# Kernel tuning notes

Hardware: AMD Instinct MI355X
Metric: run time of the kernel (lower is better)

## Reference

```python
import jax, jax.numpy as jnp
import numpy as np

B, N, F_IN, H = 1, 4096, 256, 4
OUT_F = 256
HEAD_DIM = OUT_F // H
E_RAND = 131072  # avg degree 32
LN_EPS = 1e-5


def setup_inputs() -> dict:
    key = jax.random.key(0)
    ks = jax.random.split(key, 12)
    x = jax.random.normal(ks[0], (B, N, F_IN), jnp.float32)
    # random edges + self-loops so every softmax row has at least one unmasked entry
    src = jax.random.randint(ks[1], (E_RAND,), 0, N, dtype=jnp.int32)
    dst = jax.random.randint(ks[2], (E_RAND,), 0, N, dtype=jnp.int32)
    loops = jnp.arange(N, dtype=jnp.int32)
    edge_index = jnp.stack([jnp.concatenate([loops, src]), jnp.concatenate([loops, dst])])
    s = 1.0 / np.sqrt(F_IN)
    Wq = jax.random.uniform(ks[3], (OUT_F, F_IN), jnp.float32, -s, s)
    bq = jax.random.uniform(ks[4], (OUT_F,), jnp.float32, -s, s)
    Wk = jax.random.uniform(ks[5], (OUT_F, F_IN), jnp.float32, -s, s)
    bk = jax.random.uniform(ks[6], (OUT_F,), jnp.float32, -s, s)
    Wv = jax.random.uniform(ks[7], (OUT_F, F_IN), jnp.float32, -s, s)
    bv = jax.random.uniform(ks[8], (OUT_F,), jnp.float32, -s, s)
    ln_g = jnp.ones((OUT_F,), jnp.float32)
    ln_b = jnp.zeros((OUT_F,), jnp.float32)
    return {"x": x, "edge_index": edge_index, "Wq": Wq, "bq": bq, "Wk": Wk,
            "bk": bk, "Wv": Wv, "bv": bv, "ln_g": ln_g, "ln_b": ln_b}


def _layer_norm(y, g, b):
    mu = jnp.mean(y, axis=-1, keepdims=True)
    var = jnp.mean(jnp.square(y - mu), axis=-1, keepdims=True)
    return (y - mu) * jax.lax.rsqrt(var + LN_EPS) * g + b


def reference(x, edge_index, Wq, bq, Wk, bk, Wv, bv, ln_g, ln_b):
    b, n, f_in = x.shape
    out_f = Wq.shape[0]
    hd = out_f // H
    # linear projections -> [b, H, n, hd]
    Q = (x @ Wq.T + bq).reshape(b, n, H, hd).transpose(0, 2, 1, 3)
    K = (x @ Wk.T + bk).reshape(b, n, H, hd).transpose(0, 2, 1, 3)
    V = (x @ Wv.T + bv).reshape(b, n, H, hd).transpose(0, 2, 1, 3)
    scores = jnp.einsum('bhnd,bhmd->bhnm', Q, K) / jnp.sqrt(jnp.float32(hd))
    # adjacency mask: same for every batch/head (torch scatters identically per b,h)
    adj = jnp.zeros((n, n), bool).at[edge_index[0], edge_index[1]].set(True)
    scores = jnp.where(adj, scores, -jnp.inf)
    attn = jax.nn.softmax(scores, axis=-1)  # dropout = identity (eval)
    out = jnp.einsum('bhnm,bhmd->bhnd', attn, V)
    out = out.transpose(0, 2, 1, 3).reshape(b, n, out_f)
    out = out + x if f_in == out_f else out  # residual
    out = _layer_norm(out, ln_g, ln_b)
    return (out, attn)
```

## Files before the change

### kernel.cpp

```cpp
#include <hip/hip_runtime.h>
#include <stdint.h>

#define NNODES 4096
#define FDIM 256
#define NH 4
#define HD 64
#define MWORDS 128
#define SCAP 512
#define TOTROWS (NH * NNODES)
#define ROW4 (NNODES / 4)
#define R0 5120
#define R1 13824
#define NFB 2048

typedef float f4 __attribute__((ext_vector_type(4)));

__device__ __forceinline__ void fill_zero(f4* __restrict__ attn4, size_t beg, size_t end,
                                          int fid, int t)
{
    f4 z = {0.f, 0.f, 0.f, 0.f};
    size_t stride = (size_t)NFB * 256;
    for (size_t i = beg + (size_t)fid * 256 + t; i < end; i += stride)
        attn4[i] = z;
}

__global__ __launch_bounds__(256) void k_transpose_w(
    const float* __restrict__ Wq, const float* __restrict__ Wk,
    const float* __restrict__ Wv, float* __restrict__ Wt)
{
    __shared__ float tile[32][33];
    int mat = blockIdx.z;
    const float* W = mat == 0 ? Wq : (mat == 1 ? Wk : Wv);
    float* dst = Wt + (size_t)mat * FDIM * FDIM;
    int r0 = blockIdx.y * 32, c0 = blockIdx.x * 32;
    int tx = threadIdx.x, ty = threadIdx.y;
    for (int i = ty; i < 32; i += 8)
        tile[i][tx] = W[(size_t)(r0 + i) * FDIM + c0 + tx];
    __syncthreads();
    for (int i = ty; i < 32; i += 8)
        dst[(size_t)(c0 + i) * FDIM + r0 + tx] = tile[tx][i];
}

__global__ void k_mask_build(const int* __restrict__ ei, int E, uint32_t* __restrict__ mask)
{
    int e = blockIdx.x * 256 + threadIdx.x;
    if (e >= E) return;
    int r = ei[e];
    int c = ei[E + e];
    atomicOr(&mask[(size_t)r * MWORDS + (c >> 5)], 1u << (c & 31));
}

#define TN 16
__global__ __launch_bounds__(256) void k_qkv_fill(
    const float* __restrict__ x, const float* __restrict__ Wt,
    const float* __restrict__ bq, const float* __restrict__ bk, const float* __restrict__ bv,
    float* __restrict__ qkv, float* __restrict__ attn)
{
    int t = threadIdx.x;
    if (blockIdx.x >= 3 * (NNODES / TN)) {
        fill_zero((f4*)attn, 0, (size_t)R0 * ROW4, blockIdx.x - 3 * (NNODES / TN), t);
        return;
    }
    int mat = blockIdx.x >> 8;
    int n0 = (blockIdx.x & 255) * TN;
    const float* W = Wt + (size_t)mat * FDIM * FDIM;
    const float* bias = mat == 0 ? bq : (mat == 1 ? bk : bv);
    float* dst = qkv + (size_t)mat * NNODES * FDIM;
    __shared__ float xl[TN][FDIM + 4];
    for (int f = t; f < TN * (FDIM / 4); f += 256) {
        int n = f >> 6, c4 = f & 63;
        float4 v = ((const float4*)(x + (size_t)(n0 + n) * FDIM))[c4];
        *(float4*)&xl[n][c4 * 4] = v;
    }
    __syncthreads();
    float acc[TN];
    #pragma unroll
    for (int n = 0; n < TN; ++n) acc[n] = 0.f;
    for (int k4 = 0; k4 < FDIM / 4; ++k4) {
        float w0 = W[(size_t)(k4 * 4 + 0) * FDIM + t];
        float w1 = W[(size_t)(k4 * 4 + 1) * FDIM + t];
        float w2 = W[(size_t)(k4 * 4 + 2) * FDIM + t];
        float w3 = W[(size_t)(k4 * 4 + 3) * FDIM + t];
        #pragma unroll
        for (int n = 0; n < TN; ++n) {
            float4 xv = *(const float4*)&xl[n][k4 * 4];
            acc[n] = fmaf(w0, xv.x, acc[n]);
            acc[n] = fmaf(w1, xv.y, acc[n]);
            acc[n] = fmaf(w2, xv.z, acc[n]);
            acc[n] = fmaf(w3, xv.w, acc[n]);
        }
    }
    float bb = bias[t];
    #pragma unroll
    for (int n = 0; n < TN; ++n)
        dst[(size_t)(n0 + n) * FDIM + t] = acc[n] + bb;
}

__global__ __launch_bounds__(256) void k_attn_fill(
    const float* __restrict__ qkv, const uint32_t* __restrict__ mask,
    const float* __restrict__ x, const float* __restrict__ ln_g, const float* __restrict__ ln_b,
    float* __restrict__ out, float* __restrict__ stats, float* __restrict__ attn)
{
    int t = threadIdx.x;
    if (blockIdx.x >= NNODES) {
        fill_zero((f4*)attn, (size_t)R0 * ROW4, (size_t)R1 * ROW4, blockIdx.x - NNODES, t);
        return;
    }

    const float* Q = qkv;
    const float* K = qkv + (size_t)NNODES * FDIM;
    const float* V = qkv + 2 * (size_t)NNODES * FDIM;

    __shared__ float q_lds[FDIM];
    __shared__ uint32_t mrow[MWORDS];
    __shared__ unsigned short list[NNODES];
    __shared__ float sv[NH][SCAP];
    __shared__ float red0[NH], red1[NH];
    __shared__ int cnt_s;

    int n = blockIdx.x;
    int h = t >> 6, lane = t & 63;

    q_lds[t] = Q[(size_t)n * FDIM + t];
    float xv = x[(size_t)n * FDIM + t];
    if (t < MWORDS) mrow[t] = mask[(size_t)n * MWORDS + t];
    __syncthreads();

    if (t < 64) {
        int total = 0;
        for (int r = 0; r < 2; ++r) {
            int w = r * 64 + t;
            uint32_t bits = mrow[w];
            int c = __popc(bits);
            int scan = c;
            #pragma unroll
            for (int off = 1; off < 64; off <<= 1) {
                int u = __shfl_up(scan, off);
                if (t >= off) scan += u;
            }
            int base = total + scan - c;
            while (bits) {
                int b = __ffs(bits) - 1;
                list[base++] = (unsigned short)(w * 32 + b);
                bits &= bits - 1;
            }
            total += __shfl(scan, 63);
        }
        if (t == 0) cnt_s = total;
    }
    __syncthreads();
    int cnt = cnt_s;

    const float4* qh = (const float4*)(q_lds + h * HD);

    float mi = -INFINITY, li = 0.f;
    for (int i = lane; i < cnt; i += 64) {
        int m = list[i];
        const float4* kp = (const float4*)(K + (size_t)m * FDIM + h * HD);
        float s = 0.f;
        #pragma unroll
        for (int j = 0; j < HD / 4; ++j) {
            float4 a = qh[j], b = kp[j];
            s += a.x * b.x + a.y * b.y + a.z * b.z + a.w * b.w;
        }
        s *= 0.125f;
        if (i < SCAP) sv[h][i] = s;
        float nm = fmaxf(mi, s);
        li = li * __expf(mi - nm) + __expf(s - nm);
        mi = nm;
    }
    #pragma unroll
    for (int off = 32; off; off >>= 1) {
        float mo = __shfl_xor(mi, off);
        float lo = __shfl_xor(li, off);
        float nm = fmaxf(mi, mo);
        float ea = (nm == -INFINITY) ? 0.f : __expf(mi - nm);
        float eb = (nm == -INFINITY) ? 0.f : __expf(mo - nm);
        li = li * ea + lo * eb;
        mi = nm;
    }
    float M = mi;
    float Linv = 1.f / li;
    if (lane == 0) {
        stats[((size_t)h * NNODES + n) * 2 + 0] = M;
        stats[((size_t)h * NNODES + n) * 2 + 1] = Linv;
    }

    int cm = min(cnt, SCAP);
    for (int i = lane; i < cm; i += 64)
        sv[h][i] = __expf(sv[h][i] - M) * Linv;

    const float* vb = V + (size_t)h * HD + lane;
    float o0 = 0.f, o1 = 0.f, o2 = 0.f, o3 = 0.f;
    int j = 0;
    for (; j + 3 < cm; j += 4) {
        int m0 = list[j], m1 = list[j + 1], m2 = list[j + 2], m3 = list[j + 3];
        float p0 = sv[h][j], p1 = sv[h][j + 1], p2 = sv[h][j + 2], p3 = sv[h][j + 3];
        o0 = fmaf(p0, vb[(size_t)m0 * FDIM], o0);
        o1 = fmaf(p1, vb[(size_t)m1 * FDIM], o1);
        o2 = fmaf(p2, vb[(size_t)m2 * FDIM], o2);
        o3 = fmaf(p3, vb[(size_t)m3 * FDIM], o3);
    }
    for (; j < cm; ++j)
        o0 = fmaf(sv[h][j], vb[(size_t)list[j] * FDIM], o0);
    for (; j < cnt; ++j) {
        int m = list[j];
        const float4* kp = (const float4*)(K + (size_t)m * FDIM + h * HD);
        float s = 0.f;
        #pragma unroll
        for (int jj = 0; jj < HD / 4; ++jj) {
            float4 a = qh[jj], b = kp[jj];
            s += a.x * b.x + a.y * b.y + a.z * b.z + a.w * b.w;
        }
        o0 = fmaf(__expf(s * 0.125f - M) * Linv, vb[(size_t)m * FDIM], o0);
    }
    float o = (o0 + o1) + (o2 + o3);

    float y = o + xv;
    float s1 = y, s2 = y * y;
    #pragma unroll
    for (int off = 32; off; off >>= 1) {
        s1 += __shfl_xor(s1, off);
        s2 += __shfl_xor(s2, off);
    }
    if (lane == 0) { red0[h] = s1; red1[h] = s2; }
    __syncthreads();
    float ts1 = (red0[0] + red0[1]) + (red0[2] + red0[3]);
    float ts2 = (red1[0] + red1[1]) + (red1[2] + red1[3]);
    float mu = ts1 * (1.f / 256.f);
    float var = ts2 * (1.f / 256.f) - mu * mu;
    out[(size_t)n * FDIM + t] = (y - mu) * rsqrtf(var + 1e-5f) * ln_g[t] + ln_b[t];
}

__global__ __launch_bounds__(256) void k_scatter_fill(
    const int* __restrict__ ei, int E, int nsb,
    const float* __restrict__ qkv, const float* __restrict__ stats,
    float* __restrict__ attn, int rowLo, int rowHi,
    unsigned long long fillBeg, unsigned long long fillEnd)
{
    int t = threadIdx.x;
    if (blockIdx.x >= nsb) {
        fill_zero((f4*)attn, (size_t)fillBeg, (size_t)fillEnd, blockIdx.x - nsb, t);
        return;
    }
    int idx = blockIdx.x * 256 + t;
    if (idx >= E * NH) return;
    int e = idx >> 2;
    int h = idx & 3;
    int r = ei[e];
    int c = ei[E + e];
    int row = h * NNODES + r;
    if (row < rowLo || row >= rowHi) return;

    const float* Q = qkv;
    const float* K = qkv + (size_t)NNODES * FDIM;
    const float4* qp = (const float4*)(Q + (size_t)r * FDIM + h * HD);
    const float4* kp = (const float4*)(K + (size_t)c * FDIM + h * HD);
    float s = 0.f;
    #pragma unroll
    for (int j = 0; j < HD / 4; ++j) {
        float4 a = qp[j], b = kp[j];
        s += a.x * b.x + a.y * b.y + a.z * b.z + a.w * b.w;
    }
    float M = stats[(size_t)row * 2 + 0];
    float Linv = stats[(size_t)row * 2 + 1];
    attn[(size_t)row * NNODES + c] = __expf(s * 0.125f - M) * Linv;
}

extern "C" void kernel_launch(void* const* d_in, const int* in_sizes, int n_in,
                              void* d_out, int out_size, void* d_ws, size_t ws_size,
                              hipStream_t stream)
{
    const float* x    = (const float*)d_in[0];
    const int*   ei   = (const int*)d_in[1];
    const float* Wq   = (const float*)d_in[2];
    const float* bq   = (const float*)d_in[3];
    const float* Wk   = (const float*)d_in[4];
    const float* bk   = (const float*)d_in[5];
    const float* Wv   = (const float*)d_in[6];
    const float* bv   = (const float*)d_in[7];
    const float* ln_g = (const float*)d_in[8];
    const float* ln_b = (const float*)d_in[9];
    float* out = (float*)d_out;
    float* attn = out + (size_t)NNODES * FDIM;

    int E = in_sizes[1] / 2;

    float* Wt  = (float*)d_ws;
    float* qkv = Wt + 3 * FDIM * FDIM;
    uint32_t* mask = (uint32_t*)(qkv + 3 * (size_t)NNODES * FDIM);
    float* stats = (float*)(mask + (size_t)NNODES * MWORDS);

    hipMemsetAsync(mask, 0, (size_t)NNODES * MWORDS * sizeof(uint32_t), stream);

    dim3 tb(32, 8);
    k_transpose_w<<<dim3(8, 8, 3), tb, 0, stream>>>(Wq, Wk, Wv, Wt);
    k_mask_build<<<(E + 255) / 256, 256, 0, stream>>>(ei, E, mask);

    k_qkv_fill<<<3 * (NNODES / TN) + NFB, 256, 0, stream>>>(x, Wt, bq, bk, bv, qkv, attn);

    k_attn_fill<<<NNODES + NFB, 256, 0, stream>>>(qkv, mask, x, ln_g, ln_b, out, stats, attn);

    int nsb = (E * NH + 255) / 256;
    k_scatter_fill<<<nsb + NFB, 256, 0, stream>>>(
        ei, E, nsb, qkv, stats, attn, 0, R1,
        (unsigned long long)R1 * ROW4, (unsigned long long)TOTROWS * ROW4);

    k_scatter_fill<<<nsb, 256, 0, stream>>>(
        ei, E, nsb, qkv, stats, attn, R1, TOTROWS, 0ull, 0ull);
}
```

Baseline: 211.9 us.

## Merge prep kernels and zero-fill attn with one nontemporal store per thread

Weight transpose and mask build are merged into one launch to save a kernel launch. The grid-strided zero fill of the dense attention matrix becomes one nontemporal dwordx4 store per thread, with enough fill blocks launched to cover each assigned range in a single pass. The split points between the fill ranges are also moved. This aims to cut loop overhead and cache pollution from the large zero-fill, at the cost of many more blocks and hardcoded grid sizes that must exactly cover each range.

```diff
diff --git a/kernel.cpp b/kernel.cpp
--- a/kernel.cpp
+++ b/kernel.cpp
@@ -9,45 +9,53 @@
 #define SCAP 512
 #define TOTROWS (NH * NNODES)
 #define ROW4 (NNODES / 4)
-#define R0 5120
-#define R1 13824
-#define NFB 2048
+#define R0 6144
+#define R1 14336
+#define FB3 24576
+#define FB4 32768
+#define FB5 8192
 
 typedef float f4 __attribute__((ext_vector_type(4)));
 
-__device__ __forceinline__ void fill_zero(f4* __restrict__ attn4, size_t beg, size_t end,
-                                          int fid, int t)
-{
-    f4 z = {0.f, 0.f, 0.f, 0.f};
-    size_t stride = (size_t)NFB * 256;
-    for (size_t i = beg + (size_t)fid * 256 + t; i < end; i += stride)
-        attn4[i] = z;
-}
-
-__global__ __launch_bounds__(256) void k_transpose_w(
+__device__ __forceinline__ void fill_one_nt(f4* __restrict__ base, size_t beg, size_t end,
+                                            int fid, int t)
+{
+    size_t i = beg + (size_t)fid * 256 + t;
+    if (i < end) {
+        f4 z = {0.f, 0.f, 0.f, 0.f};
+        f4* p = base + i;
+        asm volatile("global_store_dwordx4 %0, %1, off sc0 sc1 nt"
+                     :: "v"(p), "v"(z) : "memory");
+    }
+}
+
+__global__ __launch_bounds__(256) void k_prep(
     const float* __restrict__ Wq, const float* __restrict__ Wk,
-    const float* __restrict__ Wv, float* __restrict__ Wt)
+    const float* __restrict__ Wv, float* __restrict__ Wt,
+    const int* __restrict__ ei, int E, uint32_t* __restrict__ mask)
 {
     __shared__ float tile[32][33];
-    int mat = blockIdx.z;
-    const float* W = mat == 0 ? Wq : (mat == 1 ? Wk : Wv);
-    float* dst = Wt + (size_t)mat * FDIM * FDIM;
-    int r0 = blockIdx.y * 32, c0 = blockIdx.x * 32;
-    int tx = threadIdx.x, ty = threadIdx.y;
-    for (int i = ty; i < 32; i += 8)
-        tile[i][tx] = W[(size_t)(r0 + i) * FDIM + c0 + tx];
-    __syncthreads();
-    for (int i = ty; i < 32; i += 8)
-        dst[(size_t)(c0 + i) * FDIM + r0 + tx] = tile[tx][i];
-}
-
-__global__ void k_mask_build(const int* __restrict__ ei, int E, uint32_t* __restrict__ mask)
-{
-    int e = blockIdx.x * 256 + threadIdx.x;
-    if (e >= E) return;
-    int r = ei[e];
-    int c = ei[E + e];
-    atomicOr(&mask[(size_t)r * MWORDS + (c >> 5)], 1u << (c & 31));
+    int t = threadIdx.x;
+    if (blockIdx.x < 192) {
+        int mat = blockIdx.x >> 6;
+        int within = blockIdx.x & 63;
+        int c0 = (within & 7) * 32, r0 = (within >> 3) * 32;
+        const float* W = mat == 0 ? Wq : (mat == 1 ? Wk : Wv);
+        float* dst = Wt + (size_t)mat * FDIM * FDIM;
+        int tx = t & 31, ty = t >> 5;
+        for (int i = ty; i < 32; i += 8)
+            tile[i][tx] = W[(size_t)(r0 + i) * FDIM + c0 + tx];
+        __syncthreads();
+        for (int i = ty; i < 32; i += 8)
+            dst[(size_t)(c0 + i) * FDIM + r0 + tx] = tile[tx][i];
+    } else {
+        int e = (blockIdx.x - 192) * 256 + t;
+        if (e < E) {
+            int r = ei[e];
+            int c = ei[E + e];
+            atomicOr(&mask[(size_t)r * MWORDS + (c >> 5)], 1u << (c & 31));
+        }
+    }
 }
 
 #define TN 16
@@ -58,7 +66,7 @@
 {
     int t = threadIdx.x;
     if (blockIdx.x >= 3 * (NNODES / TN)) {
-        fill_zero((f4*)attn, 0, (size_t)R0 * ROW4, blockIdx.x - 3 * (NNODES / TN), t);
+        fill_one_nt((f4*)attn, 0, (size_t)R0 * ROW4, blockIdx.x - 3 * (NNODES / TN), t);
         return;
     }
     int mat = blockIdx.x >> 8;
@@ -103,7 +111,7 @@
 {
     int t = threadIdx.x;
     if (blockIdx.x >= NNODES) {
-        fill_zero((f4*)attn, (size_t)R0 * ROW4, (size_t)R1 * ROW4, blockIdx.x - NNODES, t);
+        fill_one_nt((f4*)attn, (size_t)R0 * ROW4, (size_t)R1 * ROW4, blockIdx.x - NNODES, t);
         return;
     }
 
@@ -240,7 +248,7 @@
 {
     int t = threadIdx.x;
     if (blockIdx.x >= nsb) {
-        fill_zero((f4*)attn, (size_t)fillBeg, (size_t)fillEnd, blockIdx.x - nsb, t);
+        fill_one_nt((f4*)attn, (size_t)fillBeg, (size_t)fillEnd, blockIdx.x - nsb, t);
         return;
     }
     int idx = blockIdx.x * 256 + t;
@@ -293,16 +301,15 @@
 
     hipMemsetAsync(mask, 0, (size_t)NNODES * MWORDS * sizeof(uint32_t), stream);
 
-    dim3 tb(32, 8);
-    k_transpose_w<<<dim3(8, 8, 3), tb, 0, stream>>>(Wq, Wk, Wv, Wt);
-    k_mask_build<<<(E + 255) / 256, 256, 0, stream>>>(ei, E, mask);
-
-    k_qkv_fill<<<3 * (NNODES / TN) + NFB, 256, 0, stream>>>(x, Wt, bq, bk, bv, qkv, attn);
-
-    k_attn_fill<<<NNODES + NFB, 256, 0, stream>>>(qkv, mask, x, ln_g, ln_b, out, stats, attn);
+    int nbuild = (E + 255) / 256;
+    k_prep<<<192 + nbuild, 256, 0, stream>>>(Wq, Wk, Wv, Wt, ei, E, mask);
+
+    k_qkv_fill<<<3 * (NNODES / TN) + FB3, 256, 0, stream>>>(x, Wt, bq, bk, bv, qkv, attn);
+
+    k_attn_fill<<<NNODES + FB4, 256, 0, stream>>>(qkv, mask, x, ln_g, ln_b, out, stats, attn);
 
     int nsb = (E * NH + 255) / 256;
-    k_scatter_fill<<<nsb + NFB, 256, 0, stream>>>(
+    k_scatter_fill<<<nsb + FB5, 256, 0, stream>>>(
         ei, E, nsb, qkv, stats, attn, 0, R1,
         (unsigned long long)R1 * ROW4, (unsigned long long)TOTROWS * ROW4);
 
```

Result: no change. 215.8 us (+1.8%).
